# Optimization experiments

Hardware: AMD Instinct MI355X
Metric: run time of the kernel (lower is better)

The kernel has to match this reference:

```python
import jax, jax.numpy as jnp
import numpy as np

DIM = 1024
NUM_HEADS = 16
HEAD_DIM = DIM // NUM_HEADS


def setup_inputs() -> dict:
    key = jax.random.key(0)
    ks = jax.random.split(key, 9)
    s = 1.0 / np.sqrt(DIM)
    x = jax.random.normal(ks[0], (2, 2048, DIM), dtype=jnp.float32)
    Wq = jax.random.uniform(ks[1], (DIM, DIM), jnp.float32, -s, s)
    bq = jax.random.uniform(ks[2], (DIM,), jnp.float32, -s, s)
    Wk = jax.random.uniform(ks[3], (DIM, DIM), jnp.float32, -s, s)
    bk = jax.random.uniform(ks[4], (DIM,), jnp.float32, -s, s)
    Wv = jax.random.uniform(ks[5], (DIM, DIM), jnp.float32, -s, s)
    bv = jax.random.uniform(ks[6], (DIM,), jnp.float32, -s, s)
    Wo = jax.random.uniform(ks[7], (DIM, DIM), jnp.float32, -s, s)
    bo = jax.random.uniform(ks[8], (DIM,), jnp.float32, -s, s)
    return {"x": x, "Wq": Wq, "bq": bq, "Wk": Wk, "bk": bk,
            "Wv": Wv, "bv": bv, "Wo": Wo, "bo": bo}


def reference(x, Wq, bq, Wk, bk, Wv, bv, Wo, bo):
    B, S, _ = x.shape
    # projections (torch Linear: y = x @ W.T + b); split heads -> [B, H, S, Dh]
    def split(y):
        return y.reshape(B, S, NUM_HEADS, HEAD_DIM).transpose(0, 2, 1, 3)
    q = split(x @ Wq.T + bq)
    k = split(x @ Wk.T + bk)
    v = split(x @ Wv.T + bv)
    scale = 1.0 / np.sqrt(HEAD_DIM).astype(np.float32)
    scores = jnp.einsum('bhqd,bhkd->bhqk', q, k) * scale  # [B,H,S,S]
    attn = jax.nn.softmax(scores, axis=-1)
    ctx = jnp.einsum('bhqk,bhkd->bhqd', attn, v)  # [B,H,S,Dh]
    ctx = ctx.transpose(0, 2, 1, 3).reshape(B, S, DIM)
    return ctx @ Wo.T + bo
```

## Files before the change

### kernel.cpp

```cpp
#include <hip/hip_runtime.h>
#include <hip/hip_bf16.h>
#include <math.h>

#define DIMSZ 1024
#define NHEAD 16
#define HDIM 64
#define BATCH 2
#define SEQ 2048
#define NROWS (BATCH * SEQ)

#define QSCALE 0.18033688011112042592f

typedef __attribute__((ext_vector_type(8))) _Float16 f16x8;
typedef __attribute__((ext_vector_type(2))) __fp16 fp16x2;
typedef __attribute__((ext_vector_type(4))) float f32x4;

__device__ __forceinline__ int swz(int m) { return (m ^ (m >> 2)) & 3; }

__device__ __forceinline__ ushort f2h(float x) {
    union { _Float16 h; ushort u; } cv;
    cv.h = (_Float16)x;
    return cv.u;
}

__device__ __forceinline__ unsigned pkrtz(float a, float b) {
    union { fp16x2 v; unsigned u; } c;
    c.v = __builtin_amdgcn_cvt_pkrtz(a, b);
    return c.u;
}

__device__ __forceinline__ void gld16(const void* g, void* l) {
    __builtin_amdgcn_global_load_lds((const __attribute__((address_space(1))) void*)g,
                                     (__attribute__((address_space(3))) void*)l,
                                     16, 0, 0);
}

__global__ __launch_bounds__(256) void convert_all(
    const float* __restrict__ x,
    const float* __restrict__ Wq, const float* __restrict__ Wk,
    const float* __restrict__ Wv, const float* __restrict__ Wo,
    ushort* __restrict__ Xh, ushort* __restrict__ Wh, ushort* __restrict__ Woh)
{
    const int b = blockIdx.x;
    const float* src;
    ushort* dst;
    size_t off;
    if (b < 2048)      { src = x;  dst = Xh;             off = (size_t)b * 2048; }
    else if (b < 2560) { src = Wq; dst = Wh;             off = (size_t)(b - 2048) * 2048; }
    else if (b < 3072) { src = Wk; dst = Wh + (1 << 20); off = (size_t)(b - 2560) * 2048; }
    else if (b < 3584) { src = Wv; dst = Wh + 2 * (1 << 20); off = (size_t)(b - 3072) * 2048; }
    else               { src = Wo; dst = Woh;            off = (size_t)(b - 3584) * 2048; }

    const size_t i = off + (size_t)threadIdx.x * 8;
    const float4 f0 = *(const float4*)&src[i];
    const float4 f1 = *(const float4*)&src[i + 4];
    uint4 hv;
    hv.x = (unsigned)f2h(f0.x) | ((unsigned)f2h(f0.y) << 16);
    hv.y = (unsigned)f2h(f0.z) | ((unsigned)f2h(f0.w) << 16);
    hv.z = (unsigned)f2h(f1.x) | ((unsigned)f2h(f1.y) << 16);
    hv.w = (unsigned)f2h(f1.z) | ((unsigned)f2h(f1.w) << 16);
    *(uint4*)&dst[i] = hv;
}

__global__ __launch_bounds__(256, 3) void qkv_gemm(
    const ushort* __restrict__ Xh,
    const ushort* __restrict__ Wh,
    const float* __restrict__ bq, const float* __restrict__ bk,
    const float* __restrict__ bv,
    ushort* __restrict__ Qb, ushort* __restrict__ Kb, ushort* __restrict__ Vt)
{
    __shared__ __align__(16) ushort smem[17408];

    const int tid = threadIdx.x;
    const int wave = tid >> 6;
    const int lane = tid & 63;
    const int lm = lane & 15;
    const int lq = lane >> 4;
    const int wy = wave >> 1;
    const int wx = wave & 1;
    const int m0 = blockIdx.x * 128;
    const int nbase = blockIdx.y * 128;

    const int c = tid & 3;
    const int r0 = tid >> 2;
    const int g = c ^ swz(r0 & 15);
    const ushort* gah = Xh + (size_t)(m0 + r0) * DIMSZ + g * 8;
    const ushort* gbh = Wh + (size_t)(nbase + r0) * DIMSZ + g * 8;
    const int wofs = wave * 512;

    const int fo = lm * 32 + (((lq ^ swz(lm)) & 3) << 3);
    int aofs[4], bofs[4];
#pragma unroll
    for (int i = 0; i < 4; ++i) {
        aofs[i] = (wy * 64 + i * 16) * 32 + fo;
        bofs[i] = (wx * 64 + i * 16) * 32 + fo;
    }

    f32x4 acc[4][4] = {};

    {
        gld16(gah, smem + wofs);                 gld16(gah + 64 * DIMSZ, smem + 2048 + wofs);
        gld16(gbh, smem + 4096 + wofs);          gld16(gbh + 64 * DIMSZ, smem + 6144 + wofs);
    }

    for (int kk = 0; kk < 32; ++kk) {
        __syncthreads();

        const ushort* Ah = smem;
        const ushort* Bh = smem + 4096;

        f16x8 ahf[4], bhf[4];
#pragma unroll
        for (int i = 0; i < 4; ++i) {
            ahf[i] = *(const f16x8*)&Ah[aofs[i]];
            bhf[i] = *(const f16x8*)&Bh[bofs[i]];
        }

        __syncthreads();

        if (kk + 1 < 32) {
            const int k0 = (kk + 1) * 32;
            gld16(gah + k0, smem + wofs);                 gld16(gah + 64 * DIMSZ + k0, smem + 2048 + wofs);
            gld16(gbh + k0, smem + 4096 + wofs);          gld16(gbh + 64 * DIMSZ + k0, smem + 6144 + wofs);
        }

#pragma unroll
        for (int i = 0; i < 4; ++i)
#pragma unroll
            for (int j = 0; j < 4; ++j)
                acc[i][j] = __builtin_amdgcn_mfma_f32_16x16x32_f16(ahf[i], bhf[j], acc[i][j], 0, 0, 0);
    }

    const int mat = blockIdx.y >> 3;
    const float* bias = (mat == 0) ? bq : (mat == 1) ? bk : bv;
    const int nloc0 = (blockIdx.y & 7) * 128;
    const int b = m0 >> 11;
    const int s0 = m0 & (SEQ - 1);
    ushort* sf = smem;

    __syncthreads();

    if (mat == 2) {
#pragma unroll
        for (int j = 0; j < 4; ++j) {
            const int nc = nloc0 + wx * 64 + j * 16 + lm;
            const float bb = bias[nc];
            const int d = j * 16 + lm;
#pragma unroll
            for (int i = 0; i < 4; ++i) {
                const int ss = wy * 64 + (i >> 1) * 32 + lq * 8 + (i & 1) * 4;
                ushort4 pk;
                pk.x = f2h(acc[i][j][0] + bb);
                pk.y = f2h(acc[i][j][1] + bb);
                pk.z = f2h(acc[i][j][2] + bb);
                pk.w = f2h(acc[i][j][3] + bb);
                *(ushort4*)&sf[(wx * 64 + d) * 136 + ss] = pk;
            }
        }
        __syncthreads();
#pragma unroll
        for (int p = 0; p < 8; ++p) {
            const int idx = p * 256 + tid;
            const int row = idx >> 4;
            const int hh = row >> 6;
            const int d = row & 63;
            const int sseg = (idx & 15) * 8;
            const uint4 v = *(const uint4*)&sf[row * 136 + sseg];
            const int hg = (nloc0 >> 6) + hh;
            *(uint4*)&Vt[((size_t)(b * NHEAD + hg) * HDIM + d) * SEQ + s0 + sseg] = v;
        }
    } else {
        ushort* dst = (mat == 0) ? Qb : Kb;
        const float sc = (mat == 0) ? QSCALE : 1.0f;
#pragma unroll
        for (int j = 0; j < 4; ++j) {
            const int col = wx * 64 + j * 16 + lm;
            const float bb = bias[nloc0 + col];
#pragma unroll
            for (int i = 0; i < 4; ++i) {
                const int rbase = wy * 64 + i * 16 + lq * 4;
#pragma unroll
                for (int rr = 0; rr < 4; ++rr)
                    sf[(rbase + rr) * 136 + col] = f2h((acc[i][j][rr] + bb) * sc);
            }
        }
        __syncthreads();
#pragma unroll
        for (int p = 0; p < 8; ++p) {
            const int idx = p * 256 + tid;
            const int row = idx >> 4;
            const int seg = idx & 15;
            const uint4 v = *(const uint4*)&sf[row * 136 + seg * 8];
            const int nc0 = nloc0 + seg * 8;
            const int h = nc0 >> 6;
            const int d = nc0 & 63;
            *(uint4*)&dst[((size_t)(b * NHEAD + h) * SEQ + s0 + row) * HDIM + d] = v;
        }
    }
}

__global__ __launch_bounds__(512, 4) void flash_attn_mfma(
    const ushort* __restrict__ Qb, const ushort* __restrict__ Kb,
    const ushort* __restrict__ Vt, ushort* __restrict__ CTXh)
{
    __shared__ __align__(16) ushort Ks[2][8192];
    __shared__ __align__(16) ushort Vs[2][8192];

    const int tid = threadIdx.x;
    const int w = tid >> 6;
    const int l = tid & 63;
    const int lm = l & 15;
    const int lq = l >> 4;
    const int q0 = blockIdx.x * 128;
    const int bh = blockIdx.y;

    const ushort* Kg = Kb + (size_t)bh * SEQ * HDIM;
    const ushort* Vg = Vt + (size_t)bh * HDIM * SEQ;

    const int srow_ = w * 8 + (l >> 3);
    const int sg_ = (l & 7) ^ ((l >> 3) & 7);

    f16x8 qf[2];
#pragma unroll
    for (int kt = 0; kt < 2; ++kt)
        qf[kt] = *(const f16x8*)&Qb[((size_t)bh * SEQ + q0 + w * 16 + lm) * HDIM + kt * 32 + lq * 8];

    int kbase[2], vbase[4];
#pragma unroll
    for (int kt = 0; kt < 2; ++kt)
        kbase[kt] = lm * 64 + (((kt * 4 + lq) ^ (lm & 7)) << 3);
#pragma unroll
    for (int kt2 = 0; kt2 < 4; ++kt2)
        vbase[kt2] = (kt2 >> 1) * 4096 + lm * 64 + ((((kt2 & 1) * 4 + lq) ^ (lm & 7)) << 3);

    f16x8 vones;
#pragma unroll
    for (int i = 0; i < 8; ++i) vones[i] = (_Float16)1.0f;

    f32x4 o[4] = {};
    f32x4 lacc = {};

#pragma unroll
    for (int p = 0; p < 2; ++p) {
        gld16(Kg + (size_t)(p * 64 + srow_) * HDIM + sg_ * 8, &Ks[0][0] + p * 4096 + w * 512);
        gld16(Vg + (size_t)srow_ * SEQ + p * 64 + sg_ * 8, &Vs[0][0] + p * 4096 + w * 512);
    }

    for (int ch = 0; ch < SEQ / 128; ++ch) {
        __syncthreads();

        if (ch + 1 < SEQ / 128) {
            const int kc = (ch + 1) * 128;
            ushort* kb_n = &Ks[(ch + 1) & 1][0];
            ushort* vb_n = &Vs[(ch + 1) & 1][0];
#pragma unroll
            for (int p = 0; p < 2; ++p) {
                gld16(Kg + (size_t)(kc + p * 64 + srow_) * HDIM + sg_ * 8, kb_n + p * 4096 + w * 512);
                gld16(Vg + (size_t)srow_ * SEQ + kc + p * 64 + sg_ * 8, vb_n + p * 4096 + w * 512);
            }
        }

        const ushort* kb = &Ks[ch & 1][0];
        const ushort* vb = &Vs[ch & 1][0];

        f32x4 st[8] = {};
#pragma unroll
        for (int ct = 0; ct < 8; ++ct)
#pragma unroll
            for (int kt = 0; kt < 2; ++kt) {
                const f16x8 kf = *(const f16x8*)&kb[ct * 1024 + kbase[kt]];
                st[ct] = __builtin_amdgcn_mfma_f32_16x16x32_f16(kf, qf[kt], st[ct], 0, 0, 0);
            }

#pragma unroll
        for (int ct = 0; ct < 8; ++ct)
#pragma unroll
            for (int r = 0; r < 4; ++r)
                st[ct][r] = __builtin_amdgcn_exp2f(st[ct][r]);

        f16x8 pf[4];
#pragma unroll
        for (int kt2 = 0; kt2 < 4; ++kt2) {
            union { f16x8 v; unsigned u[4]; } pk;
#pragma unroll
            for (int t = 0; t < 2; ++t) {
                pk.u[t * 2 + 0] = pkrtz(st[kt2 * 2 + t][0], st[kt2 * 2 + t][1]);
                pk.u[t * 2 + 1] = pkrtz(st[kt2 * 2 + t][2], st[kt2 * 2 + t][3]);
            }
            pf[kt2] = pk.v;
        }

#pragma unroll
        for (int kt2 = 0; kt2 < 4; ++kt2)
            lacc = __builtin_amdgcn_mfma_f32_16x16x32_f16(pf[kt2], vones, lacc, 0, 0, 0);

#pragma unroll
        for (int dt = 0; dt < 4; ++dt)
#pragma unroll
            for (int kt2 = 0; kt2 < 4; ++kt2) {
                const f16x8 vf = *(const f16x8*)&vb[dt * 1024 + vbase[kt2]];
                o[dt] = __builtin_amdgcn_mfma_f32_16x16x32_f16(pf[kt2], vf, o[dt], 0, 0, 0);
            }
    }

    const int b = bh >> 4;
    const int h = bh & 15;
#pragma unroll
    for (int r = 0; r < 4; ++r) {
        const float lr = 1.0f / lacc[r];
        const int srow2 = q0 + w * 16 + lq * 4 + r;
        const size_t base = ((size_t)b * SEQ + srow2) * DIMSZ + h * HDIM;
#pragma unroll
        for (int dt = 0; dt < 4; ++dt)
            CTXh[base + dt * 16 + lm] = f2h(o[dt][r] * lr);
    }
}

__global__ __launch_bounds__(256) void oproj_gemm(
    const ushort* __restrict__ Ah_g, const ushort* __restrict__ Bh_g,
    const float* __restrict__ bias, float* __restrict__ out)
{
    __shared__ __align__(16) ushort smem[6144];

    const int tid = threadIdx.x;
    const int wave = tid >> 6;
    const int lane = tid & 63;
    const int lm = lane & 15;
    const int lq = lane >> 4;
    const int wy = wave >> 1;
    const int wx = wave & 1;
    const int m0 = blockIdx.x * 64;
    const int n0 = blockIdx.y * 128;

    const int c = tid & 3;
    const int r0 = tid >> 2;
    const int g = c ^ swz(r0 & 15);
    const ushort* gah = Ah_g + (size_t)(m0 + r0) * DIMSZ + g * 8;
    const ushort* gbh = Bh_g + (size_t)(n0 + r0) * DIMSZ + g * 8;
    const int wofs = wave * 512;

    const int fo = lm * 32 + (((lq ^ swz(lm)) & 3) << 3);
    int aofs[2], bofs[4];
#pragma unroll
    for (int i = 0; i < 2; ++i) aofs[i] = (wy * 32 + i * 16) * 32 + fo;
#pragma unroll
    for (int j = 0; j < 4; ++j) bofs[j] = (wx * 64 + j * 16) * 32 + fo;

    f32x4 acc[2][4] = {};

    {
        gld16(gah, smem + wofs);
        gld16(gbh, smem + 2048 + wofs);   gld16(gbh + 64 * DIMSZ, smem + 4096 + wofs);
    }

    for (int kk = 0; kk < 32; ++kk) {
        __syncthreads();

        f16x8 ahf[2], bhf[4];
#pragma unroll
        for (int i = 0; i < 2; ++i) ahf[i] = *(const f16x8*)&smem[aofs[i]];
#pragma unroll
        for (int j = 0; j < 4; ++j) bhf[j] = *(const f16x8*)&smem[2048 + bofs[j]];

        __syncthreads();

        if (kk + 1 < 32) {
            const int k0 = (kk + 1) * 32;
            gld16(gah + k0, smem + wofs);
            gld16(gbh + k0, smem + 2048 + wofs);   gld16(gbh + 64 * DIMSZ + k0, smem + 4096 + wofs);
        }

#pragma unroll
        for (int i = 0; i < 2; ++i)
#pragma unroll
            for (int j = 0; j < 4; ++j)
                acc[i][j] = __builtin_amdgcn_mfma_f32_16x16x32_f16(ahf[i], bhf[j], acc[i][j], 0, 0, 0);
    }

#pragma unroll
    for (int j = 0; j < 4; ++j) {
        const int nc = n0 + wx * 64 + j * 16 + lm;
        const float bb = bias[nc];
#pragma unroll
        for (int i = 0; i < 2; ++i) {
            const int mb = m0 + wy * 32 + i * 16 + lq * 4;
#pragma unroll
            for (int rr = 0; rr < 4; ++rr)
                out[(size_t)(mb + rr) * DIMSZ + nc] = acc[i][j][rr] + bb;
        }
    }
}

extern "C" void kernel_launch(void* const* d_in, const int* in_sizes, int n_in,
                              void* d_out, int out_size, void* d_ws, size_t ws_size,
                              hipStream_t stream)
{
    const float* x  = (const float*)d_in[0];
    const float* Wq = (const float*)d_in[1];
    const float* bq = (const float*)d_in[2];
    const float* Wk = (const float*)d_in[3];
    const float* bk = (const float*)d_in[4];
    const float* Wv = (const float*)d_in[5];
    const float* bv = (const float*)d_in[6];
    const float* Wo = (const float*)d_in[7];
    const float* bo = (const float*)d_in[8];
    float* out = (float*)d_out;

    const size_t elems = (size_t)NROWS * DIMSZ;
    ushort* Qb   = (ushort*)d_ws;
    ushort* Kb   = Qb + elems;
    ushort* Vt   = Kb + elems;
    ushort* CTXh = Vt + elems;
    ushort* Wh   = CTXh + elems;
    ushort* Woh  = Wh + 3 * (1 << 20);
    ushort* Xh   = CTXh;

    convert_all<<<4096, 256, 0, stream>>>(x, Wq, Wk, Wv, Wo, Xh, Wh, Woh);

    qkv_gemm<<<dim3(32, 24), 256, 0, stream>>>(Xh, Wh, bq, bk, bv, Qb, Kb, Vt);

    flash_attn_mfma<<<dim3(SEQ / 128, BATCH * NHEAD), 512, 0, stream>>>(Qb, Kb, Vt, CTXh);

    oproj_gemm<<<dim3(64, 8), 256, 0, stream>>>(CTXh, Woh, bo, out);
}
```

Baseline: 181.9 us.

## Process two query row-tiles per wave in flash attention with 256 threads

Halves the flash-attention block to 4 waves, with each wave now handling 32 query rows (two 16-row MFMA tiles) instead of 16. Each K and V fragment read from LDS feeds two MFMAs, which halves LDS read traffic per MFMA and gives more independent MFMA chains. Each thread now issues twice as many global-to-LDS loads. The cost is roughly double the accumulator and score registers per wave, and launch bounds fall from (512,4) to (256,2), which may reduce occupancy and latency hiding.

```diff
diff --git a/kernel.cpp b/kernel.cpp
--- a/kernel.cpp
+++ b/kernel.cpp
@@ -199,7 +199,7 @@
     }
 }
 
-__global__ __launch_bounds__(512, 4) void flash_attn_mfma(
+__global__ __launch_bounds__(256, 2) void flash_attn_mfma(
     const ushort* __restrict__ Qb, const ushort* __restrict__ Kb,
     const ushort* __restrict__ Vt, ushort* __restrict__ CTXh)
 {
@@ -217,13 +217,15 @@
     const ushort* Kg = Kb + (size_t)bh * SEQ * HDIM;
     const ushort* Vg = Vt + (size_t)bh * HDIM * SEQ;
 
-    const int srow_ = w * 8 + (l >> 3);
-    const int sg_ = (l & 7) ^ ((l >> 3) & 7);
-
-    f16x8 qf[2];
-#pragma unroll
-    for (int kt = 0; kt < 2; ++kt)
-        qf[kt] = *(const f16x8*)&Qb[((size_t)bh * SEQ + q0 + w * 16 + lm) * HDIM + kt * 32 + lq * 8];
+    const int sr8 = l >> 3;
+    const int sg_ = (l & 7) ^ (sr8 & 7);
+
+    f16x8 qf[2][2];
+#pragma unroll
+    for (int rt = 0; rt < 2; ++rt)
+#pragma unroll
+        for (int kt = 0; kt < 2; ++kt)
+            qf[rt][kt] = *(const f16x8*)&Qb[((size_t)bh * SEQ + q0 + w * 32 + rt * 16 + lm) * HDIM + kt * 32 + lq * 8];
 
     int kbase[2], vbase[4];
 #pragma unroll
@@ -237,13 +239,17 @@
 #pragma unroll
     for (int i = 0; i < 8; ++i) vones[i] = (_Float16)1.0f;
 
-    f32x4 o[4] = {};
-    f32x4 lacc = {};
+    f32x4 o[2][4] = {};
+    f32x4 lacc[2] = {};
 
 #pragma unroll
     for (int p = 0; p < 2; ++p) {
-        gld16(Kg + (size_t)(p * 64 + srow_) * HDIM + sg_ * 8, &Ks[0][0] + p * 4096 + w * 512);
-        gld16(Vg + (size_t)srow_ * SEQ + p * 64 + sg_ * 8, &Vs[0][0] + p * 4096 + w * 512);
+        const int kr = p * 64 + w * 16 + sr8;
+        gld16(Kg + (size_t)kr * HDIM + sg_ * 8,        &Ks[0][0] + p * 4096 + w * 1024);
+        gld16(Kg + (size_t)(kr + 8) * HDIM + sg_ * 8,  &Ks[0][0] + p * 4096 + w * 1024 + 512);
+        const int vr = w * 16 + sr8;
+        gld16(Vg + (size_t)vr * SEQ + p * 64 + sg_ * 8,       &Vs[0][0] + p * 4096 + w * 1024);
+        gld16(Vg + (size_t)(vr + 8) * SEQ + p * 64 + sg_ * 8, &Vs[0][0] + p * 4096 + w * 1024 + 512);
     }
 
     for (int ch = 0; ch < SEQ / 128; ++ch) {
@@ -255,64 +261,78 @@
             ushort* vb_n = &Vs[(ch + 1) & 1][0];
 #pragma unroll
             for (int p = 0; p < 2; ++p) {
-                gld16(Kg + (size_t)(kc + p * 64 + srow_) * HDIM + sg_ * 8, kb_n + p * 4096 + w * 512);
-                gld16(Vg + (size_t)srow_ * SEQ + kc + p * 64 + sg_ * 8, vb_n + p * 4096 + w * 512);
+                const int kr = kc + p * 64 + w * 16 + sr8;
+                gld16(Kg + (size_t)kr * HDIM + sg_ * 8,        kb_n + p * 4096 + w * 1024);
+                gld16(Kg + (size_t)(kr + 8) * HDIM + sg_ * 8,  kb_n + p * 4096 + w * 1024 + 512);
+                const int vr = w * 16 + sr8;
+                gld16(Vg + (size_t)vr * SEQ + kc + p * 64 + sg_ * 8,       vb_n + p * 4096 + w * 1024);
+                gld16(Vg + (size_t)(vr + 8) * SEQ + kc + p * 64 + sg_ * 8, vb_n + p * 4096 + w * 1024 + 512);
             }
         }
 
         const ushort* kb = &Ks[ch & 1][0];
         const ushort* vb = &Vs[ch & 1][0];
 
-        f32x4 st[8] = {};
+        f32x4 st[2][8] = {};
 #pragma unroll
         for (int ct = 0; ct < 8; ++ct)
 #pragma unroll
             for (int kt = 0; kt < 2; ++kt) {
                 const f16x8 kf = *(const f16x8*)&kb[ct * 1024 + kbase[kt]];
-                st[ct] = __builtin_amdgcn_mfma_f32_16x16x32_f16(kf, qf[kt], st[ct], 0, 0, 0);
-            }
-
-#pragma unroll
-        for (int ct = 0; ct < 8; ++ct)
-#pragma unroll
-            for (int r = 0; r < 4; ++r)
-                st[ct][r] = __builtin_amdgcn_exp2f(st[ct][r]);
-
-        f16x8 pf[4];
+                st[0][ct] = __builtin_amdgcn_mfma_f32_16x16x32_f16(kf, qf[0][kt], st[0][ct], 0, 0, 0);
+                st[1][ct] = __builtin_amdgcn_mfma_f32_16x16x32_f16(kf, qf[1][kt], st[1][ct], 0, 0, 0);
+            }
+
+#pragma unroll
+        for (int rt = 0; rt < 2; ++rt)
+#pragma unroll
+            for (int ct = 0; ct < 8; ++ct)
+#pragma unroll
+                for (int r = 0; r < 4; ++r)
+                    st[rt][ct][r] = __builtin_amdgcn_exp2f(st[rt][ct][r]);
+
+        f16x8 pf[2][4];
+#pragma unroll
+        for (int rt = 0; rt < 2; ++rt)
+#pragma unroll
+            for (int kt2 = 0; kt2 < 4; ++kt2) {
+                union { f16x8 v; unsigned u[4]; } pk;
+#pragma unroll
+                for (int t = 0; t < 2; ++t) {
+                    pk.u[t * 2 + 0] = pkrtz(st[rt][kt2 * 2 + t][0], st[rt][kt2 * 2 + t][1]);
+                    pk.u[t * 2 + 1] = pkrtz(st[rt][kt2 * 2 + t][2], st[rt][kt2 * 2 + t][3]);
+                }
+                pf[rt][kt2] = pk.v;
+            }
+
 #pragma unroll
         for (int kt2 = 0; kt2 < 4; ++kt2) {
-            union { f16x8 v; unsigned u[4]; } pk;
-#pragma unroll
-            for (int t = 0; t < 2; ++t) {
-                pk.u[t * 2 + 0] = pkrtz(st[kt2 * 2 + t][0], st[kt2 * 2 + t][1]);
-                pk.u[t * 2 + 1] = pkrtz(st[kt2 * 2 + t][2], st[kt2 * 2 + t][3]);
-            }
-            pf[kt2] = pk.v;
-        }
-
-#pragma unroll
-        for (int kt2 = 0; kt2 < 4; ++kt2)
-            lacc = __builtin_amdgcn_mfma_f32_16x16x32_f16(pf[kt2], vones, lacc, 0, 0, 0);
+            lacc[0] = __builtin_amdgcn_mfma_f32_16x16x32_f16(pf[0][kt2], vones, lacc[0], 0, 0, 0);
+            lacc[1] = __builtin_amdgcn_mfma_f32_16x16x32_f16(pf[1][kt2], vones, lacc[1], 0, 0, 0);
+        }
 
 #pragma unroll
         for (int dt = 0; dt < 4; ++dt)
 #pragma unroll
             for (int kt2 = 0; kt2 < 4; ++kt2) {
                 const f16x8 vf = *(const f16x8*)&vb[dt * 1024 + vbase[kt2]];
-                o[dt] = __builtin_amdgcn_mfma_f32_16x16x32_f16(pf[kt2], vf, o[dt], 0, 0, 0);
+                o[0][dt] = __builtin_amdgcn_mfma_f32_16x16x32_f16(pf[0][kt2], vf, o[0][dt], 0, 0, 0);
+                o[1][dt] = __builtin_amdgcn_mfma_f32_16x16x32_f16(pf[1][kt2], vf, o[1][dt], 0, 0, 0);
             }
     }
 
     const int b = bh >> 4;
     const int h = bh & 15;
 #pragma unroll
+    for (int rt = 0; rt < 2; ++rt)
+#pragma unroll
     for (int r = 0; r < 4; ++r) {
-        const float lr = 1.0f / lacc[r];
-        const int srow2 = q0 + w * 16 + lq * 4 + r;
+        const float lr = 1.0f / lacc[rt][r];
+        const int srow2 = q0 + w * 32 + rt * 16 + lq * 4 + r;
         const size_t base = ((size_t)b * SEQ + srow2) * DIMSZ + h * HDIM;
 #pragma unroll
         for (int dt = 0; dt < 4; ++dt)
-            CTXh[base + dt * 16 + lm] = f2h(o[dt][r] * lr);
+            CTXh[base + dt * 16 + lm] = f2h(o[rt][dt][r] * lr);
     }
 }
 
@@ -419,7 +439,7 @@
 
     qkv_gemm<<<dim3(32, 24), 256, 0, stream>>>(Xh, Wh, bq, bk, bv, Qb, Kb, Vt);
 
-    flash_attn_mfma<<<dim3(SEQ / 128, BATCH * NHEAD), 512, 0, stream>>>(Qb, Kb, Vt, CTXh);
+    flash_attn_mfma<<<dim3(SEQ / 128, BATCH * NHEAD), 256, 0, stream>>>(Qb, Kb, Vt, CTXh);
 
     oproj_gemm<<<dim3(64, 8), 256, 0, stream>>>(CTXh, Woh, bo, out);
 }
```

Result: no change. 183.6 us (+0.9%).
